# Kernel optimization log

Measured on AMD Instinct MI355X. Metric: run time of the kernel, lower is better.

Reference implementation:

```python
import jax, jax.numpy as jnp
import numpy as np

N = 50000   # nodes
E = 640000  # edges
IN = 128    # input feature dim (== H*C so every layer has a residual)
H = 4       # heads
C = 32      # out channels per head
L = 3       # layers
D = H * C   # 128, per-layer output width
NEG_SLOPE = 0.2
LN_EPS = 1e-5


def setup_inputs() -> dict:
    key = jax.random.key(0)
    ks = jax.random.split(key, 6)
    s = 0.1  # keep activations well-scaled
    x = jax.random.normal(ks[0], (N, IN), dtype=jnp.float32)
    edge_index = jax.random.randint(ks[1], (2, E), 0, N)
    Wl = jax.random.normal(ks[2], (L, IN, D), dtype=jnp.float32) * s
    bl = jnp.zeros((L, D), dtype=jnp.float32)
    Wr = jax.random.normal(ks[3], (L, IN, D), dtype=jnp.float32) * s
    br = jnp.zeros((L, D), dtype=jnp.float32)
    att = jax.random.normal(ks[4], (L, H, C), dtype=jnp.float32) * s
    bias = jnp.zeros((L, D), dtype=jnp.float32)
    gamma = jnp.ones((L, D), dtype=jnp.float32)
    beta = jnp.zeros((L, D), dtype=jnp.float32)
    return {"x": x, "edge_index": edge_index, "Wl": Wl, "bl": bl,
            "Wr": Wr, "br": br, "att": att, "bias": bias,
            "gamma": gamma, "beta": beta}


def _gatv2_layer(x, src, dst, Wl, bl, Wr, br, att, bias):
    # GATv2Conv (concat heads, eval mode so attention dropout is identity)
    xl = (x @ Wl + bl).reshape(N, H, C)  # source transform
    xr = (x @ Wr + br).reshape(N, H, C)  # target transform
    # edge-wise gather: message along edge j->i uses xl[j] + xr[i]
    e = jax.nn.leaky_relu(xl[src] + xr[dst], NEG_SLOPE)      # [E,H,C]
    logit = jnp.einsum('ehc,hc->eh', e, att)                  # [E,H]
    # segment softmax over incoming edges of each target node
    m = jax.ops.segment_max(logit, dst, num_segments=N)       # [N,H]
    a = jnp.exp(logit - m[dst])
    denom = jax.ops.segment_sum(a, dst, num_segments=N)       # [N,H]
    a = a / (denom[dst] + 1e-16)
    # scatter-aggregate weighted source messages
    out = jax.ops.segment_sum(a[:, :, None] * xl[src], dst, num_segments=N)
    return out.reshape(N, D) + bias


def _layer_norm(h, g, b):
    mu = jnp.mean(h, axis=-1, keepdims=True)
    var = jnp.mean((h - mu) ** 2, axis=-1, keepdims=True)
    return (h - mu) * jax.lax.rsqrt(var + LN_EPS) * g + b


def reference(x, edge_index, Wl, bl, Wr, br, att, bias, gamma, beta):
    src, dst = edge_index[0], edge_index[1]
    out = x
    for l in range(L):  # small fixed layer count
        h = jax.nn.relu(_gatv2_layer(out, src, dst, Wl[l], bl[l], Wr[l], br[l], att[l], bias[l]))
        h = _layer_norm(h, gamma[l], beta[l])
        out = h + out  # in_dim == hidden*heads, so residual at every layer
    return out
```

## Files before the change

kernel.cpp:

```cpp
#include <hip/hip_runtime.h>
#include <hip/hip_bf16.h>
#include <math.h>

#define N_NODES 50000
#define N_EDGES 640000
#define DIM 128
#define NLAYER 3
#define LN_EPS 1e-5f
#define LOG2E 1.44269504088896f
#define NSCAN 49
#define NG2 782
#define SCATB 2500

#if __has_builtin(__builtin_amdgcn_exp2f)
#define EXP2(x) __builtin_amdgcn_exp2f(x)
#else
#define EXP2(x) exp2f(x)
#endif

typedef __attribute__((ext_vector_type(8))) short bf16x8;
typedef __attribute__((ext_vector_type(4))) float f32x4;

__device__ inline ushort f2b(float f) {
    __hip_bfloat16 h = __float2bfloat16(f);
    return *reinterpret_cast<ushort*>(&h);
}
__device__ inline float bf_lo(unsigned u) { return __uint_as_float(u << 16); }
__device__ inline float bf_hi(unsigned u) { return __uint_as_float(u & 0xffff0000u); }
__device__ inline float lr(float t) { return fmaf(0.4f, fabsf(t), 0.6f * t); }
__device__ inline unsigned pack2(float a, float b) {
    return (unsigned)f2b(a) | ((unsigned)f2b(b) << 16);
}
__device__ inline int cw_of(int w) { return (w & 15) + 32 * (w >> 4); }

template<int CTRL>
__device__ inline float dppadd(float v) {
    int m = __builtin_amdgcn_update_dpp(0, __float_as_int(v), CTRL, 0xF, 0xF, true);
    return v + __int_as_float(m);
}
__device__ inline float reduce16(float v) {
    v = dppadd<0x124>(v);
    v = dppadd<0x128>(v);
    v = dppadd<0xB1>(v);
    v = dppadd<0x4E>(v);
    return v;
}


__global__ __launch_bounds__(256) void zerofill(int4* __restrict__ p, int n4) {
    int i = blockIdx.x * 256 + threadIdx.x;
    if (i < n4) p[i] = make_int4(0, 0, 0, 0);
}


__global__ __launch_bounds__(256) void fusedinit(
    const float* __restrict__ x, unsigned* __restrict__ curb,
    const float* __restrict__ Wl, const float* __restrict__ Wr, ushort* __restrict__ Wt,
    const int* __restrict__ dst, int* __restrict__ deg,
    const float* __restrict__ att, const float* __restrict__ bias,
    const float* __restrict__ gamma, const float* __restrict__ beta,
    float2* __restrict__ params)
{
    int b = blockIdx.x, t = threadIdx.x;
    if (b < 12500) {
        int i = b * 256 + t;
        int node = i >> 6, w = i & 63;
        int c = cw_of(w);
        curb[i] = pack2(x[node * DIM + c], x[node * DIM + c + 16]);
    } else if (b < 12884) {
        int i = (b - 12500) * 256 + t;
        if (i < NLAYER * 2 * DIM * DIM) {
            int p = i & 127, n = (i >> 7) & 127, mat = (i >> 14) & 1, l = i >> 15;
            int c = cw_of(p >> 1) + (p & 1) * 16;
            const float* W = mat ? Wr : Wl;
            Wt[i] = f2b(W[l * DIM * DIM + c * DIM + n]);
        }
    } else if (b < 15384) {
        int e = (b - 12884) * 256 + t;
        atomicAdd(&deg[dst[e]], 1);
    } else {
        int i = t;
        if (i < NLAYER * 64) {
            int l = i >> 6, w = i & 63;
            int c = cw_of(w);
            const float* A = att + l * DIM;
            const float* B = bias + l * DIM;
            const float* G = gamma + l * DIM;
            const float* E = beta + l * DIM;
            params[l * 256 + w]       = make_float2(A[c] * LOG2E, A[c + 16] * LOG2E);
            params[l * 256 + 64 + w]  = make_float2(B[c], B[c + 16]);
            params[l * 256 + 128 + w] = make_float2(G[c], G[c + 16]);
            params[l * 256 + 192 + w] = make_float2(E[c], E[c + 16]);
        }
    }
}


__global__ __launch_bounds__(1024) void scan1(const int* __restrict__ deg,
                                              int* __restrict__ rowptr,
                                              int* __restrict__ bsum,
                                              int* __restrict__ blockhist) {
    __shared__ int sd[1024];
    __shared__ int lh[256];
    int t = threadIdx.x;
    int idx = blockIdx.x * 1024 + t;
    if (t < 256) lh[t] = 0;
    __syncthreads();
    int v = (idx < N_NODES) ? deg[idx] : 0;
    if (idx < N_NODES) atomicAdd(&lh[v < 255 ? v : 255], 1);
    sd[t] = v;
    __syncthreads();
    for (int off = 1; off < 1024; off <<= 1) {
        int add = (t >= off) ? sd[t - off] : 0;
        __syncthreads();
        sd[t] += add;
        __syncthreads();
    }
    if (idx < N_NODES) rowptr[idx + 1] = sd[t];
    if (t == 1023) bsum[blockIdx.x] = sd[1023];
    if (t < 256) blockhist[blockIdx.x * 256 + t] = lh[t];
}

__global__ __launch_bounds__(1024) void midscan(const int* __restrict__ bsum,
                                                int* __restrict__ bcarry,
                                                const int* __restrict__ blockhist,
                                                int* __restrict__ bboff) {
    __shared__ int sh[256];
    int t = threadIdx.x;
    if (t < 256) {
        int tot = 0;
        for (int b = 0; b < NSCAN; ++b) tot += blockhist[b * 256 + t];
        sh[t] = tot;
    }
    __syncthreads();
    for (int off = 1; off < 256; off <<= 1) {
        int add = 0;
        if (t < 256 && t >= off) add = sh[t - off];
        __syncthreads();
        if (t < 256) sh[t] += add;
        __syncthreads();
    }
    if (t < 256) {
        int run = sh[255] - sh[t];
        for (int b = 0; b < NSCAN; ++b) {
            bboff[b * 256 + t] = run;
            run += blockhist[b * 256 + t];
        }
    }
    if (t == 0) {
        int c = 0;
        for (int b = 0; b < NSCAN; ++b) { bcarry[b] = c; c += bsum[b]; }
    }
}

__global__ __launch_bounds__(1024) void scan2(int* __restrict__ rowptr,
                                              const int* __restrict__ bcarry,
                                              const int* __restrict__ deg,
                                              const int* __restrict__ bboff,
                                              int* __restrict__ order) {
    __shared__ int lh[256];
    int t = threadIdx.x;
    int idx = blockIdx.x * 1024 + t;
    if (t < 256) lh[t] = 0;
    __syncthreads();
    int carry = bcarry[blockIdx.x];
    if (idx == 0) rowptr[0] = 0;
    if (idx < N_NODES) {
        rowptr[idx + 1] += carry;
        int d = deg[idx];
        int bin = d < 255 ? d : 255;
        int rank = atomicAdd(&lh[bin], 1);
        order[bboff[blockIdx.x * 256 + bin] + rank] = idx;
    }
}


__global__ __launch_bounds__(256) void gemm_sc(
    const ushort* __restrict__ A,
    const ushort* __restrict__ Wt_l,
    const float* __restrict__ bl, const float* __restrict__ br,
    unsigned* __restrict__ xlb, unsigned* __restrict__ xrb,
    int do_scat,
    const int* __restrict__ src, const int* __restrict__ dst,
    const int* __restrict__ rowptr, int* __restrict__ cnt,
    int* __restrict__ esrc,
    const int* __restrict__ order, const int* __restrict__ deg,
    int4* __restrict__ slotinfo)
{
    __shared__ char lds[16384];
    int b = blockIdx.x, t = threadIdx.x;
    if (do_scat) {
        if (b < SCATB) {
            int e = b * 256 + t;
            int d = dst[e];
            int pos = rowptr[d] + atomicAdd(&cnt[d], 1);
            esrc[pos] = src[e] << 8;
            if (e < N_NODES) {
                int nd = order[e];
                int r0 = rowptr[nd];
                slotinfo[e] = make_int4(nd, r0, r0 + deg[nd], 0);
            }
            return;
        }
        b -= SCATB;
    }

    int mat = b & 1;
    int tile = b >> 1;
    int rowbase = tile * 64;

    int wid = t >> 6, lane = t & 63;
    int wr = wid >> 1, wc = wid & 1;
    int fr = lane & 15, kg = lane >> 4;

    const ushort* W = Wt_l + (size_t)mat * DIM * DIM;

    bf16x8 bfr[4][4];
    #pragma unroll
    for (int kf = 0; kf < 4; ++kf)
        #pragma unroll
        for (int nf = 0; nf < 4; ++nf)
            bfr[kf][nf] = *(const bf16x8*)(W + (size_t)(wc * 64 + nf * 16 + fr) * DIM
                                             + kg * 8 + kf * 32);

    const char* Ab = (const char*)A + (size_t)rowbase * 256;
    uint4 sa[4];
    #pragma unroll
    for (int i = 0; i < 4; ++i)
        sa[i] = *(const uint4*)(Ab + (i * 256 + t) * 16);
    #pragma unroll
    for (int i = 0; i < 4; ++i) {
        int o = (i * 256 + t) * 16;
        int row = o >> 8, ch = (o >> 4) & 15;
        *(uint4*)&lds[row * 256 + ((ch ^ (row & 7)) << 4)] = sa[i];
    }
    __syncthreads();

    f32x4 acc[2][4];
    #pragma unroll
    for (int mf = 0; mf < 2; ++mf)
        #pragma unroll
        for (int nf = 0; nf < 4; ++nf)
            acc[mf][nf] = (f32x4){0.f, 0.f, 0.f, 0.f};

    #pragma unroll
    for (int kf = 0; kf < 4; ++kf) {
        int c = kf * 4 + kg;
        bf16x8 af[2];
        #pragma unroll
        for (int mf = 0; mf < 2; ++mf) {
            int rl = wr * 32 + mf * 16 + fr;
            af[mf] = *(const bf16x8*)&lds[rl * 256 + ((c ^ (rl & 7)) << 4)];
        }
        #pragma unroll
        for (int mf = 0; mf < 2; ++mf)
            #pragma unroll
            for (int nf = 0; nf < 4; ++nf)
                acc[mf][nf] = __builtin_amdgcn_mfma_f32_16x16x32_bf16(
                    af[mf], bfr[kf][nf], acc[mf][nf], 0, 0, 0);
    }
    __syncthreads();

    const float* bias = mat ? br : bl;
    float bb[4];
    #pragma unroll
    for (int nf = 0; nf < 4; ++nf) bb[nf] = bias[wc * 64 + nf * 16 + fr];

    unsigned* ldsO = (unsigned*)lds;
    #pragma unroll
    for (int mf = 0; mf < 2; ++mf) {
        #pragma unroll
        for (int pj = 0; pj < 2; ++pj) {
            int w = fr + 32 * wc + 16 * pj;
            #pragma unroll
            for (int r = 0; r < 4; ++r) {
                int rl = wr * 32 + mf * 16 + kg * 4 + r;
                ldsO[rl * 64 + w] =
                    pack2(acc[mf][2 * pj][r] + bb[2 * pj],
                          acc[mf][2 * pj + 1][r] + bb[2 * pj + 1]);
            }
        }
    }
    __syncthreads();

    unsigned* out = mat ? xrb : xlb;
    char* ob = (char*)out + (size_t)rowbase * 256;
    #pragma unroll
    for (int i = 0; i < 4; ++i) {
        int o = (i * 256 + t) * 16;
        int row = rowbase + (o >> 8);
        if (row < N_NODES)
            *(uint4*)(ob + o) = *(const uint4*)&lds[o];
    }
}


__device__ inline void gather8(const char* __restrict__ xb, int laneoff,
                               const int j[8], unsigned u[8]) {
    #pragma unroll
    for (int i = 0; i < 8; ++i)
        u[i] = *(const unsigned*)(xb + j[i] + laneoff);
}

__device__ inline void compute8(const unsigned u[8], float ax, float ay,
                                float xrx, float xry,
                                float& s, float& ox, float& oy) {
    #pragma unroll
    for (int i = 0; i < 8; ++i) {
        float vx = bf_lo(u[i]), vy = bf_hi(u[i]);
        float p = lr(vx + xrx) * ax + lr(vy + xry) * ay;
        p = reduce16(p);
        float w = EXP2(p);
        s += w; ox = fmaf(w, vx, ox); oy = fmaf(w, vy, oy);
    }
}

__device__ inline void computeT(const unsigned u[8], float ax, float ay,
                                float xrx, float xry,
                                float& s, float& ox, float& oy, int rem) {
    #pragma unroll
    for (int i = 0; i < 8; ++i) {
        if (i < rem) {
            float vx = bf_lo(u[i]), vy = bf_hi(u[i]);
            float p = lr(vx + xrx) * ax + lr(vy + xry) * ay;
            p = reduce16(p);
            float w = EXP2(p);
            s += w; ox = fmaf(w, vx, ox); oy = fmaf(w, vy, oy);
        }
    }
}

__global__ __launch_bounds__(256) void agg_kernel(
    const unsigned* __restrict__ xlb2, const unsigned* __restrict__ xrb2,
    const int* __restrict__ esrc, const int4* __restrict__ slotinfo,
    const float2* __restrict__ P4,
    unsigned* __restrict__ curb, float* __restrict__ outf, int last)
{
    int slot = blockIdx.x * 4 + (threadIdx.x >> 6);
    int lane = threadIdx.x & 63;
    int4 si = slotinfo[slot];
    int node = __builtin_amdgcn_readfirstlane(si.x);
    int e0   = __builtin_amdgcn_readfirstlane(si.y);
    int e1   = __builtin_amdgcn_readfirstlane(si.z);

    unsigned xru = xrb2[node * 64 + lane];
    float2 att2 = P4[lane];
    float2 b2   = P4[64 + lane];
    float2 g2   = P4[128 + lane];
    float2 be2  = P4[192 + lane];
    unsigned old = curb[node * 64 + lane];
    float xrx = bf_lo(xru), xry = bf_hi(xru);

    const char* xb = (const char*)xlb2;
    int laneoff = lane << 2;

    float s = 0.f, ox = 0.f, oy = 0.f;
    int nb = (e1 - e0) >> 3;
    int rem = (e1 - e0) & 7;

    int jc[8], jn[8];
    unsigned uc[8], un[8];

    if (nb > 0) {
        #pragma unroll
        for (int i = 0; i < 8; ++i) jc[i] = esrc[e0 + i];
        gather8(xb, laneoff, jc, uc);
    }
    int ec = e0;
    for (int b = 1; b < nb; ++b) {
        int en = ec + 8;
        #pragma unroll
        for (int i = 0; i < 8; ++i) jn[i] = esrc[en + i];
        gather8(xb, laneoff, jn, un);
        compute8(uc, att2.x, att2.y, xrx, xry, s, ox, oy);
        #pragma unroll
        for (int i = 0; i < 8; ++i) uc[i] = un[i];
        ec = en;
    }
    if (nb > 0) {
        if (rem) {
            int et = ec + 8;
            #pragma unroll
            for (int i = 0; i < 8; ++i)
                jn[i] = esrc[et + (i < rem ? i : rem - 1)];
            gather8(xb, laneoff, jn, un);
            compute8(uc, att2.x, att2.y, xrx, xry, s, ox, oy);
            computeT(un, att2.x, att2.y, xrx, xry, s, ox, oy, rem);
        } else {
            compute8(uc, att2.x, att2.y, xrx, xry, s, ox, oy);
        }
    } else if (rem) {
        #pragma unroll
        for (int i = 0; i < 8; ++i)
            jc[i] = esrc[e0 + (i < rem ? i : rem - 1)];
        gather8(xb, laneoff, jc, uc);
        computeT(uc, att2.x, att2.y, xrx, xry, s, ox, oy, rem);
    }

    float inv = 1.f / (s + 1e-16f);
    float gx = fmaxf(fmaf(ox, inv, b2.x), 0.f);
    float gy = fmaxf(fmaf(oy, inv, b2.y), 0.f);

    float sum = gx + gy;
    sum = reduce16(sum);
    sum += __shfl_xor(sum, 16);
    sum += __shfl_xor(sum, 32);
    float mu = sum * (1.f / 128.f);
    float dx = gx - mu, dy = gy - mu;
    float ss = dx * dx + dy * dy;
    ss = reduce16(ss);
    ss += __shfl_xor(ss, 16);
    ss += __shfl_xor(ss, 32);
    float rstd = rsqrtf(ss * (1.f / 128.f) + LN_EPS);

    float yx = fmaf(dx * rstd, g2.x, be2.x) + bf_lo(old);
    float yy = fmaf(dy * rstd, g2.y, be2.y) + bf_hi(old);

    if (last) {
        int c = cw_of(lane);
        outf[node * DIM + c] = yx;
        outf[node * DIM + c + 16] = yy;
    } else {
        curb[node * 64 + lane] = pack2(yx, yy);
    }
}


extern "C" void kernel_launch(void* const* d_in, const int* in_sizes, int n_in,
                              void* d_out, int out_size, void* d_ws, size_t ws_size,
                              hipStream_t stream) {
    const float* x     = (const float*)d_in[0];
    const int*   ei    = (const int*)d_in[1];
    const float* Wl    = (const float*)d_in[2];
    const float* bl    = (const float*)d_in[3];
    const float* Wr    = (const float*)d_in[4];
    const float* br    = (const float*)d_in[5];
    const float* att   = (const float*)d_in[6];
    const float* bias  = (const float*)d_in[7];
    const float* gamma = (const float*)d_in[8];
    const float* beta  = (const float*)d_in[9];
    float* outf = (float*)d_out;

    char* ws = (char*)d_ws;
    size_t off = 0;
    auto alloc = [&](size_t bytes) -> void* {
        void* p = ws + off;
        off += (bytes + 255) & ~size_t(255);
        return p;
    };
    unsigned* curb = (unsigned*)alloc((size_t)N_NODES * 64 * 4);
    unsigned* xlb  = (unsigned*)alloc((size_t)N_NODES * 64 * 4 + 16384);
    unsigned* xrb  = (unsigned*)alloc((size_t)N_NODES * 64 * 4 + 16384);
    ushort* Wt     = (ushort*)alloc((size_t)NLAYER * 2 * DIM * DIM * 2);
    int* esrc      = (int*)alloc((size_t)N_EDGES * 4);
    int* rowptr    = (int*)alloc((size_t)(N_NODES + 1) * 4);
    int* zbase     = (int*)alloc((size_t)(2 * N_NODES + 2 * 64) * 4);
    int* deg = zbase, *cnt = zbase + N_NODES;
    int* bsum = cnt + N_NODES, *bcarry = bsum + 64;
    int* blockhist = (int*)alloc((size_t)NSCAN * 256 * 4);
    int* bboff     = (int*)alloc((size_t)NSCAN * 256 * 4);
    int* order     = (int*)alloc((size_t)N_NODES * 4);
    int4* slotinfo = (int4*)alloc((size_t)N_NODES * 16);
    float2* params = (float2*)alloc((size_t)NLAYER * 256 * sizeof(float2));

    const int* srcArr = ei;
    const int* dstArr = ei + N_EDGES;

    int n4 = (2 * N_NODES + 2 * 64) / 4;
    zerofill<<<(n4 + 255) / 256, 256, 0, stream>>>((int4*)zbase, n4);
    fusedinit<<<15385, 256, 0, stream>>>(x, curb, Wl, Wr, Wt, dstArr, deg,
                                         att, bias, gamma, beta, params);
    scan1<<<NSCAN, 1024, 0, stream>>>(deg, rowptr, bsum, blockhist);
    midscan<<<1, 1024, 0, stream>>>(bsum, bcarry, blockhist, bboff);
    scan2<<<NSCAN, 1024, 0, stream>>>(rowptr, bcarry, deg, bboff, order);

    for (int l = 0; l < NLAYER; ++l) {
        int do_scat = (l == 0) ? 1 : 0;
        int grid = 2 * NG2 + (do_scat ? SCATB : 0);
        gemm_sc<<<grid, 256, 0, stream>>>(
            (const ushort*)curb, Wt + (size_t)l * 2 * DIM * DIM,
            bl + (size_t)l * DIM, br + (size_t)l * DIM, xlb, xrb,
            do_scat, srcArr, dstArr, rowptr, cnt, esrc, order, deg, slotinfo);
        agg_kernel<<<12500, 256, 0, stream>>>(
            xlb, xrb, esrc, slotinfo, params + (size_t)l * 256,
            curb, outf, l == NLAYER - 1 ? 1 : 0);
    }
}
```

Baseline: 249.6 us.

## Make projection GEMM persistent with LDS-staged weights and double-buffered A tiles

The xl/xr projection GEMM now runs on a fixed grid of 512 blocks, and each block loops over 64-row tiles with a stride of 256 tiles. Each block copies its 128x128 bf16 weight matrix into LDS once and reads its B fragments from there, instead of every per-tile block pulling them from global memory. The next A tile is prefetched into registers during the MFMA work and written into a second LDS buffer, so loading overlaps compute. In exchange, each block now uses about 64KB of LDS, which caps blocks per CU. The layer-0 edge-scatter blocks share this kernel, so they also reserve that LDS and may run at lower occupancy.

```diff
diff --git a/kernel.cpp b/kernel.cpp
--- a/kernel.cpp
+++ b/kernel.cpp
@@ -9,7 +9,8 @@
 #define LN_EPS 1e-5f
 #define LOG2E 1.44269504088896f
 #define NSCAN 49
-#define NG2 782
+#define NT64 782
+#define GEMMB 512
 #define SCATB 2500
 
 #if __has_builtin(__builtin_amdgcn_exp2f)
@@ -187,7 +188,8 @@
     const int* __restrict__ order, const int* __restrict__ deg,
     int4* __restrict__ slotinfo)
 {
-    __shared__ char lds[16384];
+    __shared__ char ldsB[32768];
+    __shared__ char ldsA[2][16384];
     int b = blockIdx.x, t = threadIdx.x;
     if (do_scat) {
         if (b < SCATB) {
@@ -206,91 +208,117 @@
     }
 
     int mat = b & 1;
-    int tile = b >> 1;
-    int rowbase = tile * 64;
+    int bslot = b >> 1;
+    const ushort* W = Wt_l + (size_t)mat * DIM * DIM;
+
+    #pragma unroll
+    for (int i = 0; i < 8; ++i) {
+        int o = (i * 256 + t) * 16;
+        *(uint4*)&ldsB[o] = *(const uint4*)((const char*)W + o);
+    }
+    __syncthreads();
 
     int wid = t >> 6, lane = t & 63;
     int wr = wid >> 1, wc = wid & 1;
     int fr = lane & 15, kg = lane >> 4;
 
-    const ushort* W = Wt_l + (size_t)mat * DIM * DIM;
-
     bf16x8 bfr[4][4];
     #pragma unroll
     for (int kf = 0; kf < 4; ++kf)
         #pragma unroll
-        for (int nf = 0; nf < 4; ++nf)
-            bfr[kf][nf] = *(const bf16x8*)(W + (size_t)(wc * 64 + nf * 16 + fr) * DIM
-                                             + kg * 8 + kf * 32);
-
-    const char* Ab = (const char*)A + (size_t)rowbase * 256;
-    uint4 sa[4];
-    #pragma unroll
-    for (int i = 0; i < 4; ++i)
-        sa[i] = *(const uint4*)(Ab + (i * 256 + t) * 16);
-    #pragma unroll
-    for (int i = 0; i < 4; ++i) {
-        int o = (i * 256 + t) * 16;
-        int row = o >> 8, ch = (o >> 4) & 15;
-        *(uint4*)&lds[row * 256 + ((ch ^ (row & 7)) << 4)] = sa[i];
-    }
-    __syncthreads();
-
-    f32x4 acc[2][4];
-    #pragma unroll
-    for (int mf = 0; mf < 2; ++mf)
-        #pragma unroll
-        for (int nf = 0; nf < 4; ++nf)
-            acc[mf][nf] = (f32x4){0.f, 0.f, 0.f, 0.f};
-
-    #pragma unroll
-    for (int kf = 0; kf < 4; ++kf) {
-        int c = kf * 4 + kg;
-        bf16x8 af[2];
-        #pragma unroll
-        for (int mf = 0; mf < 2; ++mf) {
-            int rl = wr * 32 + mf * 16 + fr;
-            af[mf] = *(const bf16x8*)&lds[rl * 256 + ((c ^ (rl & 7)) << 4)];
-        }
-        #pragma unroll
-        for (int mf = 0; mf < 2; ++mf)
-            #pragma unroll
-            for (int nf = 0; nf < 4; ++nf)
-                acc[mf][nf] = __builtin_amdgcn_mfma_f32_16x16x32_bf16(
-                    af[mf], bfr[kf][nf], acc[mf][nf], 0, 0, 0);
-    }
-    __syncthreads();
+        for (int nf = 0; nf < 4; ++nf) {
+            int nl = wc * 64 + nf * 16 + fr;
+            bfr[kf][nf] = *(const bf16x8*)&ldsB[nl * 256 + kg * 16 + kf * 64];
+        }
 
     const float* bias = mat ? br : bl;
     float bb[4];
     #pragma unroll
     for (int nf = 0; nf < 4; ++nf) bb[nf] = bias[wc * 64 + nf * 16 + fr];
-
-    unsigned* ldsO = (unsigned*)lds;
-    #pragma unroll
-    for (int mf = 0; mf < 2; ++mf) {
-        #pragma unroll
-        for (int pj = 0; pj < 2; ++pj) {
-            int w = fr + 32 * wc + 16 * pj;
-            #pragma unroll
-            for (int r = 0; r < 4; ++r) {
-                int rl = wr * 32 + mf * 16 + kg * 4 + r;
-                ldsO[rl * 64 + w] =
-                    pack2(acc[mf][2 * pj][r] + bb[2 * pj],
-                          acc[mf][2 * pj + 1][r] + bb[2 * pj + 1]);
+    unsigned* out = mat ? xrb : xlb;
+
+    {
+        const char* Ab = (const char*)A + (size_t)bslot * 64 * 256;
+        #pragma unroll
+        for (int i = 0; i < 4; ++i) {
+            int o = (i * 256 + t) * 16;
+            uint4 v = *(const uint4*)(Ab + o);
+            int row = o >> 8, ch = (o >> 4) & 15;
+            *(uint4*)&ldsA[0][row * 256 + ((ch ^ (row & 7)) << 4)] = v;
+        }
+    }
+    __syncthreads();
+
+    int cur = 0;
+    for (int tt = bslot; tt < NT64; tt += 256) {
+        uint4 sa[4];
+        int tn = tt + 256;
+        bool havenext = tn < NT64;
+        if (havenext) {
+            const char* Ab = (const char*)A + (size_t)tn * 64 * 256;
+            #pragma unroll
+            for (int i = 0; i < 4; ++i)
+                sa[i] = *(const uint4*)(Ab + (i * 256 + t) * 16);
+        }
+
+        f32x4 acc[2][4];
+        #pragma unroll
+        for (int mf = 0; mf < 2; ++mf)
+            #pragma unroll
+            for (int nf = 0; nf < 4; ++nf)
+                acc[mf][nf] = (f32x4){0.f, 0.f, 0.f, 0.f};
+        #pragma unroll
+        for (int kf = 0; kf < 4; ++kf) {
+            int c = kf * 4 + kg;
+            bf16x8 af[2];
+            #pragma unroll
+            for (int mf = 0; mf < 2; ++mf) {
+                int rl = wr * 32 + mf * 16 + fr;
+                af[mf] = *(const bf16x8*)&ldsA[cur][rl * 256 + ((c ^ (rl & 7)) << 4)];
             }
-        }
-    }
-    __syncthreads();
-
-    unsigned* out = mat ? xrb : xlb;
-    char* ob = (char*)out + (size_t)rowbase * 256;
-    #pragma unroll
-    for (int i = 0; i < 4; ++i) {
-        int o = (i * 256 + t) * 16;
-        int row = rowbase + (o >> 8);
-        if (row < N_NODES)
-            *(uint4*)(ob + o) = *(const uint4*)&lds[o];
+            #pragma unroll
+            for (int mf = 0; mf < 2; ++mf)
+                #pragma unroll
+                for (int nf = 0; nf < 4; ++nf)
+                    acc[mf][nf] = __builtin_amdgcn_mfma_f32_16x16x32_bf16(
+                        af[mf], bfr[kf][nf], acc[mf][nf], 0, 0, 0);
+        }
+        __syncthreads();
+
+        unsigned* ldsO = (unsigned*)ldsA[cur];
+        #pragma unroll
+        for (int mf = 0; mf < 2; ++mf) {
+            #pragma unroll
+            for (int pj = 0; pj < 2; ++pj) {
+                int w = fr + 32 * wc + 16 * pj;
+                #pragma unroll
+                for (int r = 0; r < 4; ++r) {
+                    int rl = wr * 32 + mf * 16 + kg * 4 + r;
+                    ldsO[rl * 64 + w] =
+                        pack2(acc[mf][2 * pj][r] + bb[2 * pj],
+                              acc[mf][2 * pj + 1][r] + bb[2 * pj + 1]);
+                }
+            }
+        }
+        if (havenext) {
+            #pragma unroll
+            for (int i = 0; i < 4; ++i) {
+                int o = (i * 256 + t) * 16;
+                int row = o >> 8, ch = (o >> 4) & 15;
+                *(uint4*)&ldsA[cur ^ 1][row * 256 + ((ch ^ (row & 7)) << 4)] = sa[i];
+            }
+        }
+        __syncthreads();
+
+        char* ob = (char*)out + (size_t)tt * 64 * 256;
+        #pragma unroll
+        for (int i = 0; i < 4; ++i) {
+            int o = (i * 256 + t) * 16;
+            int row = tt * 64 + (o >> 8);
+            if (row < N_NODES)
+                *(uint4*)(ob + o) = *(const uint4*)&ldsA[cur][o];
+        }
+        cur ^= 1;
     }
 }
 
@@ -476,7 +504,7 @@
 
     for (int l = 0; l < NLAYER; ++l) {
         int do_scat = (l == 0) ? 1 : 0;
-        int grid = 2 * NG2 + (do_scat ? SCATB : 0);
+        int grid = GEMMB + (do_scat ? SCATB : 0);
         gemm_sc<<<grid, 256, 0, stream>>>(
             (const ushort*)curb, Wt + (size_t)l * 2 * DIM * DIM,
             bl + (size_t)l * DIM, br + (size_t)l * DIM, xlb, xrb,
```

Result: slower. 261.8 us (+4.9%).
